# Kernel optimization log

Measured on AMD Instinct MI355X. Metric: run time of the kernel, lower is better.

Reference implementation:

```python
import jax, jax.numpy as jnp
import numpy as np

EPS = 1e-7  # K.epsilon()
ROUTINGS = 3


def squash(v, axis=-1):
    s2 = jnp.sum(jnp.square(v), axis=axis, keepdims=True)
    scale = s2 / (1.0 + s2) / jnp.sqrt(s2 + EPS)
    return scale * v


def setup_inputs() -> dict:
    key = jax.random.key(0)
    kx, kw = jax.random.split(key)
    B, In, Din, Nc, Dc = 64, 2048, 16, 32, 32
    x = jax.random.normal(kx, (B, In, Din), dtype=jnp.float32)
    W = jax.random.normal(kw, (Nc, In, Dc, Din), dtype=jnp.float32) * 0.05
    return {"x": x, "W": W}


def reference(x, W):
    # x: [B, In, Din]; W: [Nc, In, Dc, Din]
    # Prediction vectors u_hat[b,i,j,d] = sum_k W[j,i,d,k] * x[b,i,k]
    # (the original tf.scan over batch + batch_dot computes exactly this,
    #  serialized; here it is a single batched einsum)
    hat = jnp.einsum('bik,jidk->bijd', x, W)  # [B, In, Nc, Dc]
    b = jnp.zeros(hat.shape[:3], dtype=hat.dtype)  # routing logits [B, In, Nc]
    v = None
    for i in range(ROUTINGS):
        c = jax.nn.softmax(b, axis=2)                 # over output capsules Nc
        s = jnp.einsum('bij,bijd->bjd', c, hat)       # weighted sum over In
        v = squash(s, axis=-1)                        # [B, Nc, Dc]
        if i < ROUTINGS - 1:
            b = b + jnp.einsum('bijd,bjd->bij', hat, v)  # agreement update
    return v
```

## Files before the change

kernel.cpp:

```cpp
#include <hip/hip_runtime.h>
#include <math.h>


#define B_TOT   64
#define IN_CAPS 2048
#define DIN     16
#define NC      32
#define DC      32
#define JD      (NC * DC)
#define B_CHUNK 16
#define I_CHUNK 16
#define N_IG    (IN_CAPS / I_CHUNK)
#define EPS_SQ  1e-7f

template <int PHASE, int ATOMIC>
__launch_bounds__(256, 2)
__global__ void caps_pass(const float* __restrict__ x,
                          const float* __restrict__ W,
                          const float* __restrict__ vsum,
                          float* __restrict__ P)
{
    __shared__ float xs[B_CHUNK][DIN];
    __shared__ float c_s[B_CHUNK][NC];
    __shared__ float hat_s[PHASE == 1 ? B_CHUNK * JD : 4];

    const int t    = threadIdx.x;
    const int j    = t >> 3;
    const int doff = (t & 7) * 4;
    const int jd0  = j * DC + doff;

    const int b0 = blockIdx.y * B_CHUNK;
    const int i0 = blockIdx.x * I_CHUNK;

    float acc[B_CHUNK][4];
#pragma unroll
    for (int b = 0; b < B_CHUNK; ++b)
#pragma unroll
        for (int dd = 0; dd < 4; ++dd) acc[b][dd] = 0.f;

    for (int il = 0; il < I_CHUNK; ++il) {
        const int i = i0 + il;

        {
            const int bl = t >> 4, k = t & 15;
            xs[bl][k] = x[((size_t)(b0 + bl) * IN_CAPS + i) * DIN + k];
        }
        __syncthreads();

        const float4* Wp =
            (const float4*)(W + (((size_t)j * IN_CAPS + i) * DC + doff) * DIN);
        float4 wreg[16];
#pragma unroll
        for (int q = 0; q < 16; ++q) wreg[q] = Wp[q];

        float lp[B_CHUNK];
#pragma unroll
        for (int b = 0; b < B_CHUNK; ++b) {
            float h[4];
#pragma unroll
            for (int dd = 0; dd < 4; ++dd) {
                float hs = 0.f;
#pragma unroll
                for (int q4 = 0; q4 < 4; ++q4) {
                    const float4 wv = wreg[dd * 4 + q4];
                    hs += wv.x * xs[b][q4 * 4 + 0];
                    hs += wv.y * xs[b][q4 * 4 + 1];
                    hs += wv.z * xs[b][q4 * 4 + 2];
                    hs += wv.w * xs[b][q4 * 4 + 3];
                }
                h[dd] = hs;
            }
            if (PHASE == 0) {
#pragma unroll
                for (int dd = 0; dd < 4; ++dd) acc[b][dd] += h[dd];
            } else {
                *(float4*)&hat_s[b * JD + jd0] = make_float4(h[0], h[1], h[2], h[3]);
                const float4 vv =
                    *(const float4*)&vsum[(size_t)(b0 + b) * JD + jd0];
                lp[b] = h[0] * vv.x + h[1] * vv.y + h[2] * vv.z + h[3] * vv.w;
            }
        }

        if (PHASE == 1) {
#pragma unroll
            for (int b = 0; b < B_CHUNK; ++b) {
                lp[b] += __shfl_xor(lp[b], 1, 8);
                lp[b] += __shfl_xor(lp[b], 2, 8);
                lp[b] += __shfl_xor(lp[b], 4, 8);
            }
            if ((t & 7) == 0) {
#pragma unroll
                for (int b = 0; b < B_CHUNK; ++b) c_s[b][j] = lp[b];
            }
            __syncthreads();

            {
                const int b  = t >> 4;
                const int jj = t & 15;
                float l0 = c_s[b][jj];
                float l1 = c_s[b][jj + 16];
                float m = fmaxf(l0, l1);
                m = fmaxf(m, __shfl_xor(m, 1, 16));
                m = fmaxf(m, __shfl_xor(m, 2, 16));
                m = fmaxf(m, __shfl_xor(m, 4, 16));
                m = fmaxf(m, __shfl_xor(m, 8, 16));
                const float e0 = __expf(l0 - m);
                const float e1 = __expf(l1 - m);
                float ssum = e0 + e1;
                ssum += __shfl_xor(ssum, 1, 16);
                ssum += __shfl_xor(ssum, 2, 16);
                ssum += __shfl_xor(ssum, 4, 16);
                ssum += __shfl_xor(ssum, 8, 16);
                const float inv = 1.f / ssum;
                c_s[b][jj]      = e0 * inv;
                c_s[b][jj + 16] = e1 * inv;
            }
            __syncthreads();

#pragma unroll
            for (int b = 0; b < B_CHUNK; ++b) {
                const float c   = c_s[b][j];
                const float4 hv = *(const float4*)&hat_s[b * JD + jd0];
                acc[b][0] += c * hv.x;
                acc[b][1] += c * hv.y;
                acc[b][2] += c * hv.z;
                acc[b][3] += c * hv.w;
            }
        } else {
            __syncthreads();
        }
    }

    const float scale = (PHASE == 0) ? (1.f / NC) : 1.f;
    if (ATOMIC) {
#pragma unroll
        for (int b = 0; b < B_CHUNK; ++b) {
            float* dst = &P[(size_t)(b0 + b) * JD + jd0];
#pragma unroll
            for (int dd = 0; dd < 4; ++dd)
                atomicAdd(dst + dd, acc[b][dd] * scale);
        }
    } else {
        float* dst = P + ((size_t)blockIdx.x * B_TOT + b0) * JD + jd0;
#pragma unroll
        for (int b = 0; b < B_CHUNK; ++b) {
            *(float4*)(dst + (size_t)b * JD) =
                make_float4(acc[b][0] * scale, acc[b][1] * scale,
                            acc[b][2] * scale, acc[b][3] * scale);
        }
    }
}

__global__ void reduce_squash(const float* __restrict__ P, int nparts,
                              float* __restrict__ VSUM,
                              float* __restrict__ OUT, int mode)
{
    const int idx = blockIdx.x * blockDim.x + threadIdx.x;
    float val = 0.f;
#pragma unroll 8
    for (int ig = 0; ig < nparts; ++ig)
        val += P[(size_t)ig * (B_TOT * JD) + idx];

    float s2 = val * val;
#pragma unroll
    for (int off = 16; off >= 1; off >>= 1)
        s2 += __shfl_xor(s2, off, 32);
    const float sc = s2 / (1.f + s2) * rsqrtf(s2 + EPS_SQ);
    const float v  = sc * val;
    if (mode == 0)      VSUM[idx] = v;
    else if (mode == 1) VSUM[idx] += v;
    else                OUT[idx] = v;
}

extern "C" void kernel_launch(void* const* d_in, const int* in_sizes, int n_in,
                              void* d_out, int out_size, void* d_ws, size_t ws_size,
                              hipStream_t stream)
{
    const float* x = (const float*)d_in[0];
    const float* W = (const float*)d_in[1];
    float* out = (float*)d_out;

    const dim3 grid(N_IG, B_TOT / B_CHUNK);
    const dim3 blk(256);

    const size_t P_elems  = (size_t)N_IG * B_TOT * JD;
    const size_t need     = (P_elems + (size_t)B_TOT * JD) * sizeof(float);

    if (ws_size >= need) {
        float* P    = (float*)d_ws;
        float* VSUM = P + P_elems;
        caps_pass<0, 0><<<grid, blk, 0, stream>>>(x, W, nullptr, P);
        reduce_squash<<<B_TOT * JD / 256, 256, 0, stream>>>(P, N_IG, VSUM, out, 0);
        caps_pass<1, 0><<<grid, blk, 0, stream>>>(x, W, VSUM, P);
        reduce_squash<<<B_TOT * JD / 256, 256, 0, stream>>>(P, N_IG, VSUM, out, 1);
        caps_pass<1, 0><<<grid, blk, 0, stream>>>(x, W, VSUM, P);
        reduce_squash<<<B_TOT * JD / 256, 256, 0, stream>>>(P, N_IG, VSUM, out, 2);
    } else {
        float* S    = (float*)d_ws;
        float* VSUM = S + (size_t)B_TOT * JD;
        const size_t sbytes = (size_t)B_TOT * JD * sizeof(float);
        hipMemsetAsync(S, 0, sbytes, stream);
        caps_pass<0, 1><<<grid, blk, 0, stream>>>(x, W, nullptr, S);
        reduce_squash<<<B_TOT * JD / 256, 256, 0, stream>>>(S, 1, VSUM, out, 0);
        hipMemsetAsync(S, 0, sbytes, stream);
        caps_pass<1, 1><<<grid, blk, 0, stream>>>(x, W, VSUM, S);
        reduce_squash<<<B_TOT * JD / 256, 256, 0, stream>>>(S, 1, VSUM, out, 1);
        hipMemsetAsync(S, 0, sbytes, stream);
        caps_pass<1, 1><<<grid, blk, 0, stream>>>(x, W, VSUM, S);
        reduce_squash<<<B_TOT * JD / 256, 256, 0, stream>>>(S, 1, VSUM, out, 2);
    }
}
```

Before: 717.9 us.

## Split routing into logits-stats pass and per-capsule accumulation with small partial buffer

Each routing iteration now first runs a logits kernel that recomputes hat and stores only the per-(b,i) softmax max and inverse sum, then an accumulation kernel where each block owns one output capsule j and an i-range, recomputing hat and the logit to form the coupling coefficient directly. Partial sums are reduced in-block across wavefronts, so only four partial slices are written instead of one per input-capsule group. This removes the large hat shared-memory staging and the huge partial buffer reduction, at the cost of computing hat twice per routing iteration and adding a kernel launch.

```diff
diff --git a/kernel.cpp b/kernel.cpp
--- a/kernel.cpp
+++ b/kernel.cpp
@@ -8,54 +8,271 @@
 #define NC      32
 #define DC      32
 #define JD      (NC * DC)
-#define B_CHUNK 16
-#define I_CHUNK 16
-#define N_IG    (IN_CAPS / I_CHUNK)
+#define ISPLIT  4
+#define I_PER   (IN_CAPS / ISPLIT)
+#define STEPS   (I_PER / 32)
 #define EPS_SQ  1e-7f
 
-template <int PHASE, int ATOMIC>
+__device__ __forceinline__ float dot4(float4 a, float4 b) {
+    return a.x * b.x + a.y * b.y + a.z * b.z + a.w * b.w;
+}
+
+template <int UNIFORM>
 __launch_bounds__(256, 2)
-__global__ void caps_pass(const float* __restrict__ x,
-                          const float* __restrict__ W,
-                          const float* __restrict__ vsum,
-                          float* __restrict__ P)
+__global__ void caps_accum(const float* __restrict__ x,
+                           const float* __restrict__ W,
+                           const float* __restrict__ vsum,
+                           const float* __restrict__ MD,
+                           float* __restrict__ P)
 {
-    __shared__ float xs[B_CHUNK][DIN];
-    __shared__ float c_s[B_CHUNK][NC];
-    __shared__ float hat_s[PHASE == 1 ? B_CHUNK * JD : 4];
+    __shared__ float xs[16 * 640];
+
+    const int t   = threadIdx.x;
+    const int dqi = t & 7;
+    const int io  = t >> 3;
+    const int dq  = dqi * 4;
+
+    const int bid = blockIdx.x;
+    const int j   = bid & 31;
+    const int isp = (bid >> 5) & 3;
+    const int bc  = bid >> 7;
+    const int b0  = bc * 16;
+    const int i_origin = isp * I_PER;
+
+    const float*  Wj = W + (size_t)j * IN_CAPS * (DC * DIN);
+    const float4* xg = (const float4*)x;
+
+    float acc[16][4];
+#pragma unroll
+    for (int b = 0; b < 16; ++b)
+#pragma unroll
+        for (int dd = 0; dd < 4; ++dd) acc[b][dd] = 0.f;
+
+    for (int s = 0; s < STEPS; ++s) {
+        const int ib = i_origin + s * 32;
+        __syncthreads();
+#pragma unroll
+        for (int r = 0; r < 8; ++r) {
+            const int idx  = r * 256 + t;
+            const int bb   = idx >> 7;
+            const int rest = idx & 127;
+            const int il   = rest >> 2, kq = rest & 3;
+            const float4 v = xg[(size_t)(b0 + bb) * (IN_CAPS * DIN / 4)
+                                + (size_t)ib * 4 + rest];
+            *(float4*)&xs[bb * 640 + il * 20 + kq * 4] = v;
+        }
+        __syncthreads();
+
+        const int i = ib + io;
+        const float4* Wp = (const float4*)(Wj + ((size_t)i * DC + dq) * DIN);
+        float4 w[16];
+#pragma unroll
+        for (int q = 0; q < 16; ++q) w[q] = Wp[q];
+
+#pragma unroll
+        for (int b = 0; b < 16; ++b) {
+            const float4 xv0 = *(const float4*)&xs[b * 640 + io * 20 + 0];
+            const float4 xv1 = *(const float4*)&xs[b * 640 + io * 20 + 4];
+            const float4 xv2 = *(const float4*)&xs[b * 640 + io * 20 + 8];
+            const float4 xv3 = *(const float4*)&xs[b * 640 + io * 20 + 12];
+            float h[4];
+#pragma unroll
+            for (int dd = 0; dd < 4; ++dd) {
+                h[dd] = dot4(w[dd * 4 + 0], xv0) + dot4(w[dd * 4 + 1], xv1)
+                      + dot4(w[dd * 4 + 2], xv2) + dot4(w[dd * 4 + 3], xv3);
+            }
+            if (UNIFORM) {
+#pragma unroll
+                for (int dd = 0; dd < 4; ++dd) acc[b][dd] += h[dd];
+            } else {
+                const float4 vv =
+                    *(const float4*)&vsum[((size_t)(b0 + b) * NC + j) * DC + dq];
+                float lp = h[0] * vv.x + h[1] * vv.y + h[2] * vv.z + h[3] * vv.w;
+                lp += __shfl_xor(lp, 1, 8);
+                lp += __shfl_xor(lp, 2, 8);
+                lp += __shfl_xor(lp, 4, 8);
+                const float2 md =
+                    *(const float2*)&MD[((size_t)(b0 + b) * IN_CAPS + i) * 2];
+                const float c = __expf(lp - md.x) * md.y;
+#pragma unroll
+                for (int dd = 0; dd < 4; ++dd) acc[b][dd] += c * h[dd];
+            }
+        }
+    }
+
+#pragma unroll
+    for (int b = 0; b < 16; ++b)
+#pragma unroll
+        for (int dd = 0; dd < 4; ++dd) {
+            float v = acc[b][dd];
+            v += __shfl_xor(v, 8, 64);
+            v += __shfl_xor(v, 16, 64);
+            v += __shfl_xor(v, 32, 64);
+            acc[b][dd] = v;
+        }
+
+    __syncthreads();
+    const int w_id = t >> 6, l = t & 63;
+    if (l < 8) {
+#pragma unroll
+        for (int b = 0; b < 16; ++b)
+            *(float4*)&xs[w_id * 512 + b * 32 + dq] =
+                make_float4(acc[b][0], acc[b][1], acc[b][2], acc[b][3]);
+    }
+    __syncthreads();
+
+    const float scale = UNIFORM ? (1.f / NC) : 1.f;
+#pragma unroll
+    for (int e = 0; e < 2; ++e) {
+        const int idx = e * 256 + t;
+        const float v = xs[idx] + xs[512 + idx] + xs[1024 + idx] + xs[1536 + idx];
+        const int b = idx >> 5, d = idx & 31;
+        P[((size_t)isp * B_TOT + b0 + b) * JD + j * DC + d] = v * scale;
+    }
+}
+
+__launch_bounds__(256, 2)
+__global__ void caps_logits(const float* __restrict__ x,
+                            const float* __restrict__ W,
+                            const float* __restrict__ vsum,
+                            float* __restrict__ MD)
+{
+    __shared__ float xsa[16][DIN];
+    __shared__ float ls[16][NC];
+
+    const int t   = threadIdx.x;
+    const int j   = t >> 3;
+    const int dqi = t & 7;
+    const int dq  = dqi * 4;
+
+    const int b0 = blockIdx.y * 16;
+    const int i0 = blockIdx.x * 16;
+
+    float4 vv[16];
+#pragma unroll
+    for (int b = 0; b < 16; ++b)
+        vv[b] = *(const float4*)&vsum[((size_t)(b0 + b) * NC + j) * DC + dq];
+
+    for (int il = 0; il < 16; ++il) {
+        const int i = i0 + il;
+        {
+            const int bl = t >> 4, k = t & 15;
+            xsa[bl][k] = x[((size_t)(b0 + bl) * IN_CAPS + i) * DIN + k];
+        }
+        __syncthreads();
+
+        const float4* Wp =
+            (const float4*)(W + (((size_t)j * IN_CAPS + i) * DC + dq) * DIN);
+        float4 w[16];
+#pragma unroll
+        for (int q = 0; q < 16; ++q) w[q] = Wp[q];
+
+#pragma unroll
+        for (int b = 0; b < 16; ++b) {
+            const float4 xv0 = *(const float4*)&xsa[b][0];
+            const float4 xv1 = *(const float4*)&xsa[b][4];
+            const float4 xv2 = *(const float4*)&xsa[b][8];
+            const float4 xv3 = *(const float4*)&xsa[b][12];
+            float h[4];
+#pragma unroll
+            for (int dd = 0; dd < 4; ++dd) {
+                h[dd] = dot4(w[dd * 4 + 0], xv0) + dot4(w[dd * 4 + 1], xv1)
+                      + dot4(w[dd * 4 + 2], xv2) + dot4(w[dd * 4 + 3], xv3);
+            }
+            float lp = h[0] * vv[b].x + h[1] * vv[b].y
+                     + h[2] * vv[b].z + h[3] * vv[b].w;
+            lp += __shfl_xor(lp, 1, 8);
+            lp += __shfl_xor(lp, 2, 8);
+            lp += __shfl_xor(lp, 4, 8);
+            if (dqi == 0) ls[b][j] = lp;
+        }
+        __syncthreads();
+
+        {
+            const int bb = t >> 4;
+            const int jj = t & 15;
+            const float l0 = ls[bb][jj];
+            const float l1 = ls[bb][jj + 16];
+            float m = fmaxf(l0, l1);
+            m = fmaxf(m, __shfl_xor(m, 1, 16));
+            m = fmaxf(m, __shfl_xor(m, 2, 16));
+            m = fmaxf(m, __shfl_xor(m, 4, 16));
+            m = fmaxf(m, __shfl_xor(m, 8, 16));
+            float ssum = __expf(l0 - m) + __expf(l1 - m);
+            ssum += __shfl_xor(ssum, 1, 16);
+            ssum += __shfl_xor(ssum, 2, 16);
+            ssum += __shfl_xor(ssum, 4, 16);
+            ssum += __shfl_xor(ssum, 8, 16);
+            if (jj == 0) {
+                *(float2*)&MD[((size_t)(b0 + bb) * IN_CAPS + i) * 2] =
+                    make_float2(m, 1.f / ssum);
+            }
+        }
+        __syncthreads();
+    }
+}
+
+__global__ void reduce_squash(const float* __restrict__ P, int nparts,
+                              float* __restrict__ VSUM,
+                              float* __restrict__ OUT, int mode)
+{
+    const int idx = blockIdx.x * blockDim.x + threadIdx.x;
+    float val = 0.f;
+#pragma unroll 4
+    for (int ig = 0; ig < nparts; ++ig)
+        val += P[(size_t)ig * (B_TOT * JD) + idx];
+
+    float s2 = val * val;
+#pragma unroll
+    for (int off = 16; off >= 1; off >>= 1)
+        s2 += __shfl_xor(s2, off, 32);
+    const float sc = s2 / (1.f + s2) * rsqrtf(s2 + EPS_SQ);
+    const float v  = sc * val;
+    if (mode == 0)      VSUM[idx] = v;
+    else if (mode == 1) VSUM[idx] += v;
+    else                OUT[idx] = v;
+}
+
+template <int PHASE>
+__launch_bounds__(256, 2)
+__global__ void caps_pass_atomic(const float* __restrict__ x,
+                                 const float* __restrict__ W,
+                                 const float* __restrict__ vsum,
+                                 float* __restrict__ S)
+{
+    __shared__ float xs[16][DIN];
+    __shared__ float c_s[16][NC];
+    __shared__ float hat_s[PHASE == 1 ? 16 * JD : 4];
 
     const int t    = threadIdx.x;
     const int j    = t >> 3;
     const int doff = (t & 7) * 4;
     const int jd0  = j * DC + doff;
-
-    const int b0 = blockIdx.y * B_CHUNK;
-    const int i0 = blockIdx.x * I_CHUNK;
-
-    float acc[B_CHUNK][4];
-#pragma unroll
-    for (int b = 0; b < B_CHUNK; ++b)
+    const int b0 = blockIdx.y * 16;
+    const int i0 = blockIdx.x * 16;
+
+    float acc[16][4];
+#pragma unroll
+    for (int b = 0; b < 16; ++b)
 #pragma unroll
         for (int dd = 0; dd < 4; ++dd) acc[b][dd] = 0.f;
 
-    for (int il = 0; il < I_CHUNK; ++il) {
+    for (int il = 0; il < 16; ++il) {
         const int i = i0 + il;
-
         {
             const int bl = t >> 4, k = t & 15;
             xs[bl][k] = x[((size_t)(b0 + bl) * IN_CAPS + i) * DIN + k];
         }
         __syncthreads();
-
         const float4* Wp =
             (const float4*)(W + (((size_t)j * IN_CAPS + i) * DC + doff) * DIN);
         float4 wreg[16];
 #pragma unroll
         for (int q = 0; q < 16; ++q) wreg[q] = Wp[q];
 
-        float lp[B_CHUNK];
-#pragma unroll
-        for (int b = 0; b < B_CHUNK; ++b) {
+        float lp[16];
+#pragma unroll
+        for (int b = 0; b < 16; ++b) {
             float h[4];
 #pragma unroll
             for (int dd = 0; dd < 4; ++dd) {
@@ -75,25 +292,24 @@
                 for (int dd = 0; dd < 4; ++dd) acc[b][dd] += h[dd];
             } else {
                 *(float4*)&hat_s[b * JD + jd0] = make_float4(h[0], h[1], h[2], h[3]);
-                const float4 vv =
+                const float4 vvl =
                     *(const float4*)&vsum[(size_t)(b0 + b) * JD + jd0];
-                lp[b] = h[0] * vv.x + h[1] * vv.y + h[2] * vv.z + h[3] * vv.w;
+                lp[b] = h[0] * vvl.x + h[1] * vvl.y + h[2] * vvl.z + h[3] * vvl.w;
             }
         }
 
         if (PHASE == 1) {
 #pragma unroll
-            for (int b = 0; b < B_CHUNK; ++b) {
+            for (int b = 0; b < 16; ++b) {
                 lp[b] += __shfl_xor(lp[b], 1, 8);
                 lp[b] += __shfl_xor(lp[b], 2, 8);
                 lp[b] += __shfl_xor(lp[b], 4, 8);
             }
             if ((t & 7) == 0) {
 #pragma unroll
-                for (int b = 0; b < B_CHUNK; ++b) c_s[b][j] = lp[b];
+                for (int b = 0; b < 16; ++b) c_s[b][j] = lp[b];
             }
             __syncthreads();
-
             {
                 const int b  = t >> 4;
                 const int jj = t & 15;
@@ -116,9 +332,8 @@
                 c_s[b][jj + 16] = e1 * inv;
             }
             __syncthreads();
-
-#pragma unroll
-            for (int b = 0; b < B_CHUNK; ++b) {
+#pragma unroll
+            for (int b = 0; b < 16; ++b) {
                 const float c   = c_s[b][j];
                 const float4 hv = *(const float4*)&hat_s[b * JD + jd0];
                 acc[b][0] += c * hv.x;
@@ -132,44 +347,13 @@
     }
 
     const float scale = (PHASE == 0) ? (1.f / NC) : 1.f;
-    if (ATOMIC) {
-#pragma unroll
-        for (int b = 0; b < B_CHUNK; ++b) {
-            float* dst = &P[(size_t)(b0 + b) * JD + jd0];
-#pragma unroll
-            for (int dd = 0; dd < 4; ++dd)
-                atomicAdd(dst + dd, acc[b][dd] * scale);
-        }
-    } else {
-        float* dst = P + ((size_t)blockIdx.x * B_TOT + b0) * JD + jd0;
-#pragma unroll
-        for (int b = 0; b < B_CHUNK; ++b) {
-            *(float4*)(dst + (size_t)b * JD) =
-                make_float4(acc[b][0] * scale, acc[b][1] * scale,
-                            acc[b][2] * scale, acc[b][3] * scale);
-        }
-    }
-}
-
-__global__ void reduce_squash(const float* __restrict__ P, int nparts,
-                              float* __restrict__ VSUM,
-                              float* __restrict__ OUT, int mode)
-{
-    const int idx = blockIdx.x * blockDim.x + threadIdx.x;
-    float val = 0.f;
-#pragma unroll 8
-    for (int ig = 0; ig < nparts; ++ig)
-        val += P[(size_t)ig * (B_TOT * JD) + idx];
-
-    float s2 = val * val;
-#pragma unroll
-    for (int off = 16; off >= 1; off >>= 1)
-        s2 += __shfl_xor(s2, off, 32);
-    const float sc = s2 / (1.f + s2) * rsqrtf(s2 + EPS_SQ);
-    const float v  = sc * val;
-    if (mode == 0)      VSUM[idx] = v;
-    else if (mode == 1) VSUM[idx] += v;
-    else                OUT[idx] = v;
+#pragma unroll
+    for (int b = 0; b < 16; ++b) {
+        float* dst = &S[(size_t)(b0 + b) * JD + jd0];
+#pragma unroll
+        for (int dd = 0; dd < 4; ++dd)
+            atomicAdd(dst + dd, acc[b][dd] * scale);
+    }
 }
 
 extern "C" void kernel_launch(void* const* d_in, const int* in_sizes, int n_in,
@@ -180,33 +364,39 @@
     const float* W = (const float*)d_in[1];
     float* out = (float*)d_out;
 
-    const dim3 grid(N_IG, B_TOT / B_CHUNK);
-    const dim3 blk(256);
-
-    const size_t P_elems  = (size_t)N_IG * B_TOT * JD;
-    const size_t need     = (P_elems + (size_t)B_TOT * JD) * sizeof(float);
+    const size_t P_elems  = (size_t)ISPLIT * B_TOT * JD;
+    const size_t V_elems  = (size_t)B_TOT * JD;
+    const size_t MD_elems = (size_t)B_TOT * IN_CAPS * 2;
+    const size_t need = (P_elems + V_elems + MD_elems) * sizeof(float);
 
     if (ws_size >= need) {
         float* P    = (float*)d_ws;
         float* VSUM = P + P_elems;
-        caps_pass<0, 0><<<grid, blk, 0, stream>>>(x, W, nullptr, P);
-        reduce_squash<<<B_TOT * JD / 256, 256, 0, stream>>>(P, N_IG, VSUM, out, 0);
-        caps_pass<1, 0><<<grid, blk, 0, stream>>>(x, W, VSUM, P);
-        reduce_squash<<<B_TOT * JD / 256, 256, 0, stream>>>(P, N_IG, VSUM, out, 1);
-        caps_pass<1, 0><<<grid, blk, 0, stream>>>(x, W, VSUM, P);
-        reduce_squash<<<B_TOT * JD / 256, 256, 0, stream>>>(P, N_IG, VSUM, out, 2);
+        float* MD   = VSUM + V_elems;
+
+        caps_accum<1><<<512, 256, 0, stream>>>(x, W, nullptr, nullptr, P);
+        reduce_squash<<<B_TOT * JD / 256, 256, 0, stream>>>(P, ISPLIT, VSUM, out, 0);
+
+        caps_logits<<<dim3(128, 4), 256, 0, stream>>>(x, W, VSUM, MD);
+        caps_accum<0><<<512, 256, 0, stream>>>(x, W, VSUM, MD, P);
+        reduce_squash<<<B_TOT * JD / 256, 256, 0, stream>>>(P, ISPLIT, VSUM, out, 1);
+
+        caps_logits<<<dim3(128, 4), 256, 0, stream>>>(x, W, VSUM, MD);
+        caps_accum<0><<<512, 256, 0, stream>>>(x, W, VSUM, MD, P);
+        reduce_squash<<<B_TOT * JD / 256, 256, 0, stream>>>(P, ISPLIT, VSUM, out, 2);
     } else {
         float* S    = (float*)d_ws;
-        float* VSUM = S + (size_t)B_TOT * JD;
-        const size_t sbytes = (size_t)B_TOT * JD * sizeof(float);
+        float* VSUM = S + V_elems;
+        const dim3 grid(128, 4), blk(256);
+        const size_t sbytes = V_elems * sizeof(float);
         hipMemsetAsync(S, 0, sbytes, stream);
-        caps_pass<0, 1><<<grid, blk, 0, stream>>>(x, W, nullptr, S);
+        caps_pass_atomic<0><<<grid, blk, 0, stream>>>(x, W, nullptr, S);
         reduce_squash<<<B_TOT * JD / 256, 256, 0, stream>>>(S, 1, VSUM, out, 0);
         hipMemsetAsync(S, 0, sbytes, stream);
-        caps_pass<1, 1><<<grid, blk, 0, stream>>>(x, W, VSUM, S);
+        caps_pass_atomic<1><<<grid, blk, 0, stream>>>(x, W, VSUM, S);
         reduce_squash<<<B_TOT * JD / 256, 256, 0, stream>>>(S, 1, VSUM, out, 1);
         hipMemsetAsync(S, 0, sbytes, stream);
-        caps_pass<1, 1><<<grid, blk, 0, stream>>>(x, W, VSUM, S);
+        caps_pass_atomic<1><<<grid, blk, 0, stream>>>(x, W, VSUM, S);
         reduce_squash<<<B_TOT * JD / 256, 256, 0, stream>>>(S, 1, VSUM, out, 2);
     }
 }
```

After: 1.819 ms. 153% more time.
